# Performance work log

Hardware: AMD Instinct MI355X
Metric: run time of the kernel (lower is better)

## Reference

```python
import jax, jax.numpy as jnp
import numpy as np

D_MODEL = 128
N_HEADS = 8
D_K = D_MODEL // N_HEADS
N_NODES = 50000
N_EDGES = 800000


def setup_inputs() -> dict:
    key = jax.random.key(0)
    ks = jax.random.split(key, 8)
    X = jax.random.normal(ks[0], (N_NODES, D_MODEL), dtype=jnp.float32)
    nbr_src = jax.random.randint(ks[1], (N_EDGES,), 0, N_NODES, dtype=jnp.int32)
    nbr_dst = jax.random.randint(ks[2], (N_EDGES,), 0, N_NODES, dtype=jnp.int32)
    s = 1.0 / np.sqrt(D_MODEL)
    W_qkv = jax.random.normal(ks[3], (3 * D_MODEL, D_MODEL), dtype=jnp.float32) * s
    w_bias = jax.random.normal(ks[4], (N_HEADS, D_MODEL), dtype=jnp.float32) * s
    W_gate = jax.random.normal(ks[5], (D_MODEL, D_MODEL), dtype=jnp.float32) * s
    b_gate = jax.random.normal(ks[6], (D_MODEL,), dtype=jnp.float32) * s
    W_o = jax.random.normal(ks[7], (D_MODEL, D_MODEL), dtype=jnp.float32) * s
    return {"X": X, "W_qkv": W_qkv, "w_bias": w_bias, "W_gate": W_gate,
            "b_gate": b_gate, "W_o": W_o, "nbr_src": nbr_src,
            "nbr_dst": nbr_dst, "num_cells": N_NODES}


def segment_softmax(scores, seg, num_segments):
    # scores: [E, H], seg: [E] -> softmax over edges sharing the same seg id
    mx = jax.ops.segment_max(scores, seg, num_segments=num_segments)  # [N, H]
    mx = jnp.where(jnp.isfinite(mx), mx, -1e9)
    exp_s = jnp.exp(scores - mx[seg])
    sm = jax.ops.segment_sum(exp_s, seg, num_segments=num_segments)  # [N, H]
    return exp_s / (sm[seg] + 1e-12)


def reference(X, W_qkv, w_bias, W_gate, b_gate, W_o, nbr_src, nbr_dst, num_cells):
    H, dk = N_HEADS, D_K
    scale = 1.0 / np.sqrt(dk)
    qkv = (X @ W_qkv.T).reshape(-1, 3, H, dk)      # [N, 3, H, dk]
    Q, K, V = qkv[:, 0], qkv[:, 1], qkv[:, 2]
    gate = jax.nn.sigmoid(X @ W_gate.T + b_gate).reshape(-1, H, dk)
    bias = X @ w_bias.T                             # [N, H]
    scores = jnp.einsum('ehd,ehd->eh', Q[nbr_src], K[nbr_dst]) * scale + bias[nbr_src]
    attn = segment_softmax(scores, nbr_src, num_cells)          # [E, H]
    out = jax.ops.segment_sum(attn[:, :, None] * V[nbr_dst], nbr_src,
                              num_segments=num_cells)           # [N, H, dk]
    return (gate * out).reshape(-1, D_MODEL) @ W_o.T
```

## Files before the change

### kernel.cpp

```cpp
#include <hip/hip_runtime.h>
#include <hip/hip_fp16.h>

#define DM 128
#define NHEADS 8
#define MAXDEG 64
#define SROW 136

typedef _Float16 half8 __attribute__((ext_vector_type(8)));
typedef _Float16 half2v __attribute__((ext_vector_type(2)));
typedef float floatx4 __attribute__((ext_vector_type(4)));

union H8 { half8 v; half2v h2[4]; _Float16 h[8]; };

__global__ __launch_bounds__(256) void proj_csr(
    const float* __restrict__ X, const float* __restrict__ Wqkv,
    const float* __restrict__ Wgate, const float* __restrict__ wbias,
    const float* __restrict__ b_gate,
    const int* __restrict__ nsrc, const int* __restrict__ ndst,
    int* __restrict__ cnt, int* __restrict__ csr_dst,
    _Float16* __restrict__ Q, _Float16* __restrict__ KV,
    _Float16* __restrict__ gate, float* __restrict__ bias,
    int M, int E, int P) {
  __shared__ _Float16 As[128 * SROW];
  __shared__ _Float16 Bs[64 * SROW];
  int tid = threadIdx.x;
  int bid = blockIdx.x;

  if (bid >= P) {
    int e = (bid - P) * 256 + tid;
    if (e < E) {
      int s = nsrc[e];
      int d = ndst[e];
      int p = atomicAdd(&cnt[s], 1);
      if (p < MAXDEG) csr_dst[(size_t)s * MAXDEG + p] = d;
    }
    return;
  }

  int m0 = bid * 128;

#pragma unroll
  for (int i = 0; i < 4; i++) {
    int u = tid + i * 256;
    int r = u >> 3;
    int cc = (u & 7) * 16;
    int gr = m0 + r;
    float4 f0, f1, f2, f3;
    if (gr < M) {
      const float4* src = (const float4*)(X + (size_t)gr * 128 + cc);
      f0 = src[0]; f1 = src[1]; f2 = src[2]; f3 = src[3];
    } else {
      f0 = f1 = f2 = f3 = make_float4(0.f, 0.f, 0.f, 0.f);
    }
    half8 h0 = {(_Float16)f0.x, (_Float16)f0.y, (_Float16)f0.z, (_Float16)f0.w,
                (_Float16)f1.x, (_Float16)f1.y, (_Float16)f1.z, (_Float16)f1.w};
    half8 h1 = {(_Float16)f2.x, (_Float16)f2.y, (_Float16)f2.z, (_Float16)f2.w,
                (_Float16)f3.x, (_Float16)f3.y, (_Float16)f3.z, (_Float16)f3.w};
    *(half8*)(As + r * SROW + cc) = h0;
    *(half8*)(As + r * SROW + cc + 8) = h1;
  }

  int wid = tid >> 6, lane = tid & 63;
  int quad = lane >> 4, l16 = lane & 15;
  int mw = wid * 32;

  for (int c = 0; c < 9; c++) {
    __syncthreads();
#pragma unroll
    for (int i = 0; i < 4; i++) {
      int u = tid + i * 256;
      int r = u >> 4;
      int cc = (u & 15) * 8;
      int grow = c * 64 + r;
      const float* src = nullptr;
      if (grow < 384)      src = Wqkv + (size_t)grow * 128 + cc;
      else if (grow < 512) src = Wgate + (size_t)(grow - 384) * 128 + cc;
      else if (grow < 520) src = wbias + (size_t)(grow - 512) * 128 + cc;
      half8 h = {};
      if (src) {
        float4 f0 = ((const float4*)src)[0];
        float4 f1 = ((const float4*)src)[1];
        h = half8{(_Float16)f0.x, (_Float16)f0.y, (_Float16)f0.z, (_Float16)f0.w,
                  (_Float16)f1.x, (_Float16)f1.y, (_Float16)f1.z, (_Float16)f1.w};
      }
      *(half8*)(Bs + r * SROW + cc) = h;
    }
    __syncthreads();

    floatx4 acc[2][4] = {};
#pragma unroll
    for (int kc = 0; kc < 4; kc++) {
      int ko = kc * 32 + quad * 8;
      half8 a0 = *(const half8*)(As + (mw + l16) * SROW + ko);
      half8 a1 = *(const half8*)(As + (mw + 16 + l16) * SROW + ko);
      half8 b[4];
#pragma unroll
      for (int ni = 0; ni < 4; ni++)
        b[ni] = *(const half8*)(Bs + (ni * 16 + l16) * SROW + ko);
#pragma unroll
      for (int ni = 0; ni < 4; ni++) {
        acc[0][ni] = __builtin_amdgcn_mfma_f32_16x16x32_f16(a0, b[ni], acc[0][ni], 0, 0, 0);
        acc[1][ni] = __builtin_amdgcn_mfma_f32_16x16x32_f16(a1, b[ni], acc[1][ni], 0, 0, 0);
      }
    }

    if (c == 8) {
      if (l16 < 8) {
#pragma unroll
        for (int mi = 0; mi < 2; mi++)
#pragma unroll
          for (int r = 0; r < 4; r++) {
            int row = m0 + mw + mi * 16 + quad * 4 + r;
            if (row < M) bias[(size_t)row * 8 + l16] = acc[mi][0][r];
          }
      }
    } else {
      int reg = c >> 1;
#pragma unroll
      for (int mi = 0; mi < 2; mi++) {
#pragma unroll
        for (int ni = 0; ni < 4; ni++) {
          int colL = (c & 1) * 64 + ni * 16 + l16;
#pragma unroll
          for (int r = 0; r < 4; r++) {
            int row = m0 + mw + mi * 16 + quad * 4 + r;
            if (row >= M) continue;
            float v = acc[mi][ni][r];
            if (reg == 0)      Q[(size_t)row * 128 + colL] = (_Float16)v;
            else if (reg == 1) KV[(size_t)row * 256 + colL] = (_Float16)v;
            else if (reg == 2) KV[(size_t)row * 256 + 128 + colL] = (_Float16)v;
            else gate[(size_t)row * 128 + colL] =
                   (_Float16)(1.0f / (1.0f + __expf(-(v + b_gate[colL]))));
          }
        }
      }
    }
  }
}

__global__ __launch_bounds__(256) void attn_out(
    const int* __restrict__ cnt, const int* __restrict__ csr_dst,
    const _Float16* __restrict__ Q, const _Float16* __restrict__ KV,
    const float* __restrict__ bias, const _Float16* __restrict__ gate,
    const float* __restrict__ Wo, float* __restrict__ out, int N) {
  __shared__ _Float16 Ws[64 * SROW];
  __shared__ _Float16 Gs[32 * SROW];
  int tid = threadIdx.x;
  int wid = tid >> 6, lane = tid & 63;
  int qtr = lane >> 4, l16 = lane & 15;
  int ch0 = l16 * 8;
  int n0 = blockIdx.x * 32;

  for (int i = 0; i < 8; i++) {
    int slot = wid * 8 + i;
    int n = n0 + slot;
    bool active = n < N;
    int n_eff = active ? n : 0;
    int deg = active ? cnt[n_eff] : 0;
    if (deg > MAXDEG) deg = MAXDEG;

    int dstv = csr_dst[(size_t)n_eff * MAXDEG + lane];

    H8 qu; qu.v = *(const half8*)(Q + (size_t)n_eff * DM + ch0);
    float bias_h = bias[(size_t)n_eff * NHEADS + (l16 >> 1)];

    float acc[8] = {};
    float den = 0.f;
    int iters = (deg + 3) >> 2;

    H8 kc, vc; kc.v = half8{}; vc.v = half8{};
    bool bc = false;
    if (iters > 0) {
      bc = qtr < deg;
      int d = __shfl(dstv, qtr);
      d = bc ? d : 0;
      const _Float16* kvp = KV + (size_t)d * 256 + ch0;
      kc.v = *(const half8*)kvp;
      vc.v = *(const half8*)(kvp + 128);
    }
    for (int it = 0; it < iters; it++) {
      H8 kn, vn; kn.v = half8{}; vn.v = half8{};
      bool bn = false;
      if (it + 1 < iters) {
        int e = (it + 1) * 4 + qtr;
        bn = e < deg;
        int d = __shfl(dstv, e);
        d = bn ? d : 0;
        const _Float16* kvp = KV + (size_t)d * 256 + ch0;
        kn.v = *(const half8*)kvp;
        vn.v = *(const half8*)(kvp + 128);
      }
      float p = 0.f;
#pragma unroll
      for (int j = 0; j < 4; j++)
        p = __builtin_amdgcn_fdot2(qu.h2[j], kc.h2[j], p, false);
      p += __shfl_xor(p, 1);
      float w = __expf(p * 0.25f + bias_h);
      if (!bc) w = 0.f;
      den += w;
#pragma unroll
      for (int j = 0; j < 8; j++) acc[j] = fmaf(w, (float)vc.h[j], acc[j]);
      kc = kn; vc = vn; bc = bn;
    }
#pragma unroll
    for (int j = 0; j < 8; j++) {
      acc[j] += __shfl_xor(acc[j], 16);
      acc[j] += __shfl_xor(acc[j], 32);
    }
    den += __shfl_xor(den, 16);
    den += __shfl_xor(den, 32);

    if (qtr == 0) {
      float inv = 1.0f / (den + 1e-12f);
      H8 gv; gv.v = *(const half8*)(gate + (size_t)n_eff * DM + ch0);
      half8 o;
#pragma unroll
      for (int j = 0; j < 8; j++)
        o[j] = active ? (_Float16)(acc[j] * inv * (float)gv.h[j]) : (_Float16)0.f;
      *(half8*)(Gs + slot * SROW + ch0) = o;
    }
  }

  __syncthreads();

#pragma unroll
  for (int chunk = 0; chunk < 2; chunk++) {
    if (chunk) __syncthreads();
#pragma unroll
    for (int i2 = 0; i2 < 4; i2++) {
      int u = tid + i2 * 256;
      int r = u >> 4;
      int cc = (u & 15) * 8;
      const float4* s = (const float4*)(Wo + (size_t)(chunk * 64 + r) * 128 + cc);
      float4 f0 = s[0], f1 = s[1];
      half8 h = {(_Float16)f0.x, (_Float16)f0.y, (_Float16)f0.z, (_Float16)f0.w,
                 (_Float16)f1.x, (_Float16)f1.y, (_Float16)f1.z, (_Float16)f1.w};
      *(half8*)(Ws + r * SROW + cc) = h;
    }
    __syncthreads();

    floatx4 oc[2] = {};
#pragma unroll
    for (int kc2 = 0; kc2 < 4; kc2++) {
      int ko = kc2 * 32 + qtr * 8;
      half8 b = *(const half8*)(Ws + (wid * 16 + l16) * SROW + ko);
#pragma unroll
      for (int mi = 0; mi < 2; mi++) {
        half8 a = *(const half8*)(Gs + (mi * 16 + l16) * SROW + ko);
        oc[mi] = __builtin_amdgcn_mfma_f32_16x16x32_f16(a, b, oc[mi], 0, 0, 0);
      }
    }
    int col = chunk * 64 + wid * 16 + l16;
#pragma unroll
    for (int mi = 0; mi < 2; mi++)
#pragma unroll
      for (int r = 0; r < 4; r++) {
        int row = n0 + mi * 16 + qtr * 4 + r;
        if (row < N) out[(size_t)row * 128 + col] = oc[mi][r];
      }
  }
}

extern "C" void kernel_launch(void* const* d_in, const int* in_sizes, int n_in,
                              void* d_out, int out_size, void* d_ws, size_t ws_size,
                              hipStream_t stream) {
  const float* X     = (const float*)d_in[0];
  const float* Wqkv  = (const float*)d_in[1];
  const float* wbias = (const float*)d_in[2];
  const float* Wgate = (const float*)d_in[3];
  const float* bgate = (const float*)d_in[4];
  const float* Wo    = (const float*)d_in[5];
  const int*   nsrc  = (const int*)d_in[6];
  const int*   ndst  = (const int*)d_in[7];
  int N = in_sizes[0] / 128;
  int E = in_sizes[6];
  float* out = (float*)d_out;

  char* p = (char*)d_ws;
  _Float16* Q16     = (_Float16*)p; p += (size_t)N * 128 * sizeof(_Float16);
  _Float16* KV16    = (_Float16*)p; p += (size_t)N * 256 * sizeof(_Float16);
  _Float16* gate16  = (_Float16*)p; p += (size_t)N * 128 * sizeof(_Float16);
  float* bias       = (float*)p;    p += (size_t)N * 8 * sizeof(float);
  int* cnt          = (int*)p;      p += (size_t)N * sizeof(int);
  int* csr_dst      = (int*)p;      p += (size_t)N * MAXDEG * sizeof(int);

  hipMemsetAsync(cnt, 0, (size_t)N * sizeof(int), stream);

  int P = (N + 127) / 128;
  int C = (E + 255) / 256;
  proj_csr<<<P + C, 256, 0, stream>>>(X, Wqkv, Wgate, wbias, bgate, nsrc, ndst,
                                      cnt, csr_dst, Q16, KV16, gate16, bias, N, E, P);

  attn_out<<<(N + 31) / 32, 256, 0, stream>>>(cnt, csr_dst, Q16, KV16, bias,
                                              gate16, Wo, out, N);
}
```

Measured before the change: 238.7 us.

## Load X and Wo fragments straight from global memory instead of staging through LDS

In the projection kernel, the X tile is no longer staged in shared memory. Each lane loads its MFMA A-fragment directly from global memory and converts it to fp16 in registers, once per each of the 9 weight chunks. In the output kernel, the Wo B-fragments are also read directly from global memory, which drops the LDS staging buffer and its two barriers. The CSR build now processes 4 edges per thread with the loads hoisted before the atomics, so fewer blocks are launched. This trades LDS traffic and lower LDS occupancy limits for repeated global/L2 reads of X (nine times per tile) and repeated fp32-to-fp16 conversions.

```diff
diff --git a/kernel.cpp b/kernel.cpp
--- a/kernel.cpp
+++ b/kernel.cpp
@@ -11,6 +11,11 @@
 typedef float floatx4 __attribute__((ext_vector_type(4)));
 
 union H8 { half8 v; half2v h2[4]; _Float16 h[8]; };
+
+__device__ inline half8 cvt8(const float4 f0, const float4 f1) {
+  return half8{(_Float16)f0.x, (_Float16)f0.y, (_Float16)f0.z, (_Float16)f0.w,
+               (_Float16)f1.x, (_Float16)f1.y, (_Float16)f1.z, (_Float16)f1.w};
+}
 
 __global__ __launch_bounds__(256) void proj_csr(
     const float* __restrict__ X, const float* __restrict__ Wqkv,
@@ -21,48 +26,39 @@
     _Float16* __restrict__ Q, _Float16* __restrict__ KV,
     _Float16* __restrict__ gate, float* __restrict__ bias,
     int M, int E, int P) {
-  __shared__ _Float16 As[128 * SROW];
   __shared__ _Float16 Bs[64 * SROW];
   int tid = threadIdx.x;
   int bid = blockIdx.x;
 
   if (bid >= P) {
-    int e = (bid - P) * 256 + tid;
-    if (e < E) {
-      int s = nsrc[e];
-      int d = ndst[e];
-      int p = atomicAdd(&cnt[s], 1);
-      if (p < MAXDEG) csr_dst[(size_t)s * MAXDEG + p] = d;
+    int ebase = (bid - P) * 1024 + tid;
+    int s[4], d[4];
+#pragma unroll
+    for (int j = 0; j < 4; j++) {
+      int e = ebase + j * 256;
+      bool v = e < E;
+      s[j] = v ? nsrc[e] : -1;
+      d[j] = v ? ndst[e] : 0;
+    }
+#pragma unroll
+    for (int j = 0; j < 4; j++) {
+      if (s[j] >= 0) {
+        int p = atomicAdd(&cnt[s[j]], 1);
+        if (p < MAXDEG) csr_dst[(size_t)s[j] * MAXDEG + p] = d[j];
+      }
     }
     return;
   }
 
   int m0 = bid * 128;
-
-#pragma unroll
-  for (int i = 0; i < 4; i++) {
-    int u = tid + i * 256;
-    int r = u >> 3;
-    int cc = (u & 7) * 16;
-    int gr = m0 + r;
-    float4 f0, f1, f2, f3;
-    if (gr < M) {
-      const float4* src = (const float4*)(X + (size_t)gr * 128 + cc);
-      f0 = src[0]; f1 = src[1]; f2 = src[2]; f3 = src[3];
-    } else {
-      f0 = f1 = f2 = f3 = make_float4(0.f, 0.f, 0.f, 0.f);
-    }
-    half8 h0 = {(_Float16)f0.x, (_Float16)f0.y, (_Float16)f0.z, (_Float16)f0.w,
-                (_Float16)f1.x, (_Float16)f1.y, (_Float16)f1.z, (_Float16)f1.w};
-    half8 h1 = {(_Float16)f2.x, (_Float16)f2.y, (_Float16)f2.z, (_Float16)f2.w,
-                (_Float16)f3.x, (_Float16)f3.y, (_Float16)f3.z, (_Float16)f3.w};
-    *(half8*)(As + r * SROW + cc) = h0;
-    *(half8*)(As + r * SROW + cc + 8) = h1;
-  }
-
   int wid = tid >> 6, lane = tid & 63;
   int quad = lane >> 4, l16 = lane & 15;
   int mw = wid * 32;
+
+  int ra0 = m0 + mw + l16;      if (ra0 > M - 1) ra0 = M - 1;
+  int ra1 = m0 + mw + 16 + l16; if (ra1 > M - 1) ra1 = M - 1;
+  const float* xp0 = X + (size_t)ra0 * 128 + quad * 8;
+  const float* xp1 = X + (size_t)ra1 * 128 + quad * 8;
 
   for (int c = 0; c < 9; c++) {
     __syncthreads();
@@ -77,12 +73,7 @@
       else if (grow < 512) src = Wgate + (size_t)(grow - 384) * 128 + cc;
       else if (grow < 520) src = wbias + (size_t)(grow - 512) * 128 + cc;
       half8 h = {};
-      if (src) {
-        float4 f0 = ((const float4*)src)[0];
-        float4 f1 = ((const float4*)src)[1];
-        h = half8{(_Float16)f0.x, (_Float16)f0.y, (_Float16)f0.z, (_Float16)f0.w,
-                  (_Float16)f1.x, (_Float16)f1.y, (_Float16)f1.z, (_Float16)f1.w};
-      }
+      if (src) h = cvt8(((const float4*)src)[0], ((const float4*)src)[1]);
       *(half8*)(Bs + r * SROW + cc) = h;
     }
     __syncthreads();
@@ -90,13 +81,13 @@
     floatx4 acc[2][4] = {};
 #pragma unroll
     for (int kc = 0; kc < 4; kc++) {
-      int ko = kc * 32 + quad * 8;
-      half8 a0 = *(const half8*)(As + (mw + l16) * SROW + ko);
-      half8 a1 = *(const half8*)(As + (mw + 16 + l16) * SROW + ko);
+      int ko = kc * 32;
+      half8 a0 = cvt8(((const float4*)(xp0 + ko))[0], ((const float4*)(xp0 + ko))[1]);
+      half8 a1 = cvt8(((const float4*)(xp1 + ko))[0], ((const float4*)(xp1 + ko))[1]);
       half8 b[4];
 #pragma unroll
       for (int ni = 0; ni < 4; ni++)
-        b[ni] = *(const half8*)(Bs + (ni * 16 + l16) * SROW + ko);
+        b[ni] = *(const half8*)(Bs + (ni * 16 + l16) * SROW + ko + quad * 8);
 #pragma unroll
       for (int ni = 0; ni < 4; ni++) {
         acc[0][ni] = __builtin_amdgcn_mfma_f32_16x16x32_f16(a0, b[ni], acc[0][ni], 0, 0, 0);
@@ -143,7 +134,6 @@
     const _Float16* __restrict__ Q, const _Float16* __restrict__ KV,
     const float* __restrict__ bias, const _Float16* __restrict__ gate,
     const float* __restrict__ Wo, float* __restrict__ out, int N) {
-  __shared__ _Float16 Ws[64 * SROW];
   __shared__ _Float16 Gs[32 * SROW];
   int tid = threadIdx.x;
   int wid = tid >> 6, lane = tid & 63;
@@ -225,32 +215,19 @@
 
 #pragma unroll
   for (int chunk = 0; chunk < 2; chunk++) {
-    if (chunk) __syncthreads();
-#pragma unroll
-    for (int i2 = 0; i2 < 4; i2++) {
-      int u = tid + i2 * 256;
-      int r = u >> 4;
-      int cc = (u & 15) * 8;
-      const float4* s = (const float4*)(Wo + (size_t)(chunk * 64 + r) * 128 + cc);
-      float4 f0 = s[0], f1 = s[1];
-      half8 h = {(_Float16)f0.x, (_Float16)f0.y, (_Float16)f0.z, (_Float16)f0.w,
-                 (_Float16)f1.x, (_Float16)f1.y, (_Float16)f1.z, (_Float16)f1.w};
-      *(half8*)(Ws + r * SROW + cc) = h;
-    }
-    __syncthreads();
-
+    int col = chunk * 64 + wid * 16 + l16;
+    const float* wp = Wo + (size_t)col * 128 + qtr * 8;
     floatx4 oc[2] = {};
 #pragma unroll
     for (int kc2 = 0; kc2 < 4; kc2++) {
-      int ko = kc2 * 32 + qtr * 8;
-      half8 b = *(const half8*)(Ws + (wid * 16 + l16) * SROW + ko);
+      int ko = kc2 * 32;
+      half8 b = cvt8(((const float4*)(wp + ko))[0], ((const float4*)(wp + ko))[1]);
 #pragma unroll
       for (int mi = 0; mi < 2; mi++) {
-        half8 a = *(const half8*)(Gs + (mi * 16 + l16) * SROW + ko);
+        half8 a = *(const half8*)(Gs + (mi * 16 + l16) * SROW + ko + qtr * 8);
         oc[mi] = __builtin_amdgcn_mfma_f32_16x16x32_f16(a, b, oc[mi], 0, 0, 0);
       }
     }
-    int col = chunk * 64 + wid * 16 + l16;
 #pragma unroll
     for (int mi = 0; mi < 2; mi++)
 #pragma unroll
@@ -287,7 +264,7 @@
   hipMemsetAsync(cnt, 0, (size_t)N * sizeof(int), stream);
 
   int P = (N + 127) / 128;
-  int C = (E + 255) / 256;
+  int C = (E + 1023) / 1024;
   proj_csr<<<P + C, 256, 0, stream>>>(X, Wqkv, Wgate, wbias, bgate, nsrc, ndst,
                                       cnt, csr_dst, Q16, KV16, gate16, bias, N, E, P);
 
```

New measurement: 237.0 us. About the same (-0.7%).
